# Kernel optimization log

Measured on AMD Instinct MI355X. Metric: run time of the kernel, lower is better.

The kernel has to match this reference:

```python
import jax, jax.numpy as jnp
import numpy as np

B, QL, KL, D, H = 2, 512, 8192, 1024, 8
HD = D // H  # head dim = 128


def setup_inputs() -> dict:
    key = jax.random.key(0)
    ks = jax.random.split(key, 12)
    s = 0.02
    return {
        "inputs_q": jax.random.normal(ks[0], (B, QL, D), jnp.float32),
        "inputs_k": jax.random.normal(ks[1], (B, KL, D), jnp.float32),
        "inputs_v": jax.random.normal(ks[2], (B, KL, D), jnp.float32),
        "attention_mask": jax.random.randint(ks[3], (B, QL, KL), 0, 2).astype(bool),
        "Wq": jax.random.normal(ks[4], (D, D), jnp.float32) * s,
        "bq": jnp.zeros((D,), jnp.float32),
        "Wk": jax.random.normal(ks[5], (D, D), jnp.float32) * s,
        "bk": jnp.zeros((D,), jnp.float32),
        "Wv": jax.random.normal(ks[6], (D, D), jnp.float32) * s,
        "bv": jnp.zeros((D,), jnp.float32),
        "Wf": jax.random.normal(ks[7], (D, D), jnp.float32) * s,
        "bf": jnp.zeros((D,), jnp.float32),
    }


def reference(inputs_q, inputs_k, inputs_v, attention_mask, Wq, bq, Wk, bk, Wv, bv, Wf, bf):
    # Projections (torch Linear: x @ W.T + b)
    q = inputs_q @ Wq.T + bq  # [B, QL, D]
    k = inputs_k @ Wk.T + bk  # [B, KL, D]
    v = inputs_v @ Wv.T + bv  # [B, KL, D]

    q = q.reshape(B, QL, H, HD)
    k = k.reshape(B, KL, H, HD)
    v = v.reshape(B, KL, H, HD)

    # scores [B, H, QL, KL]
    scores = jnp.einsum("bqhd,bkhd->bhqk", q, k)
    scale = 1.0 / np.sqrt(HD).astype(np.float32)
    scores = scores * scale
    large_k = jnp.float32(1e30)
    scores = jnp.where(attention_mask[:, None, :, :], scores, -large_k)

    probs = jax.nn.softmax(scores, axis=-1)
    # note: original calls self.dropout(normalized) but discards the result -> no-op

    summed = jnp.einsum("bhqk,bkhd->bqhd", probs, v).reshape(B, QL, H * HD)

    # wipe rows whose mask is all zero
    wipe = jnp.all(~attention_mask, axis=2, keepdims=True)  # [B, QL, 1]
    summed = jnp.where(wipe, jnp.zeros_like(summed), summed)

    return summed @ Wf.T + bf
```

## Files before the change

### kernel.cpp

```cpp
#include <hip/hip_runtime.h>
#include <hip/hip_bf16.h>
#include <math.h>

typedef __attribute__((ext_vector_type(4))) float fx4;
typedef __attribute__((ext_vector_type(4))) short sx4;
typedef __attribute__((ext_vector_type(8))) short sx8;
typedef unsigned long long u64;

#define MFMA16(a, b, c) __builtin_amdgcn_mfma_f32_16x16x16bf16_1k(a, b, c, 0, 0, 0)
#define MFMA32(a, b, c) __builtin_amdgcn_mfma_f32_16x16x32_bf16(a, b, c, 0, 0, 0)

__device__ __forceinline__ unsigned short f2bf(float f) {
  unsigned int u = __float_as_uint(f);
  return (unsigned short)((u + 0x7fffu + ((u >> 16) & 1u)) >> 16);
}

typedef const __attribute__((address_space(1))) char* gc1p;
typedef __attribute__((address_space(3))) char* lc3p;
__device__ __forceinline__ void glds16(const void* g, const void* lds_uniform) {
  gc1p gp = (gc1p)(unsigned long long)(uintptr_t)g;
  lc3p lp = (lc3p)(unsigned)__builtin_amdgcn_readfirstlane((int)(unsigned)(uintptr_t)lds_uniform);
  __builtin_amdgcn_global_load_lds(gp, lp, 16, 0, 0);
}

__global__ __launch_bounds__(256) void k_conv(const float* __restrict__ s,
                                              short* __restrict__ d) {
  size_t i = ((size_t)blockIdx.x * 256 + threadIdx.x) * 8;
  const fx4 a = *(const fx4*)(s + i);
  const fx4 b = *(const fx4*)(s + i + 4);
  sx8 o;
  o[0] = (short)f2bf(a[0]); o[1] = (short)f2bf(a[1]);
  o[2] = (short)f2bf(a[2]); o[3] = (short)f2bf(a[3]);
  o[4] = (short)f2bf(b[0]); o[5] = (short)f2bf(b[1]);
  o[6] = (short)f2bf(b[2]); o[7] = (short)f2bf(b[3]);
  *(sx8*)(d + i) = o;
}

__global__ __launch_bounds__(256) void k_conv_a(const float* ink, const float* inq,
                                                const float* Wq, const float* Wk,
                                                const float* Wv, const float* Wf,
                                                short* ck, short* cq, short* cwq,
                                                short* cwk, short* cwv, short* cwf) {
  int bx = blockIdx.x;
  const float* s;
  short* d;
  size_t i;
  if (bx < 8192) {
    s = ink; d = ck; i = (size_t)bx * 2048;
  } else {
    const int r = bx - 8192;
    const int seg = r >> 9;
    s = seg == 0 ? inq : seg == 1 ? Wq : seg == 2 ? Wk : seg == 3 ? Wv : Wf;
    d = seg == 0 ? cq : seg == 1 ? cwq : seg == 2 ? cwk : seg == 3 ? cwv : cwf;
    i = (size_t)(r & 511) * 2048;
  }
  i += (size_t)threadIdx.x * 8;
  const fx4 a = *(const fx4*)(s + i);
  const fx4 b = *(const fx4*)(s + i + 4);
  sx8 o;
  o[0] = (short)f2bf(a[0]); o[1] = (short)f2bf(a[1]);
  o[2] = (short)f2bf(a[2]); o[3] = (short)f2bf(a[3]);
  o[4] = (short)f2bf(b[0]); o[5] = (short)f2bf(b[1]);
  o[6] = (short)f2bf(b[2]); o[7] = (short)f2bf(b[3]);
  *(sx8*)(d + i) = o;
}

__global__ __launch_bounds__(256) void k_pack_mask(const int* __restrict__ mask,
                                                   u64* __restrict__ mb) {
  int g = blockIdx.x * 256 + threadIdx.x;
  u64 bal = __ballot(mask[g] != 0);
  if ((threadIdx.x & 63) == 0) mb[g >> 6] = bal;
}

template <int MODE>
__global__ __launch_bounds__(256) void k_gemm(const short* __restrict__ A,
                                              const short* __restrict__ Bw,
                                              const float* __restrict__ bias,
                                              void* __restrict__ Cptr,
                                              int M, int N, int K, float alpha) {
  __shared__ __align__(16) short sA[8192];
  __shared__ __align__(16) short sB[8192];
  const int t = threadIdx.x;
  const int lane = t & 63;
  const int w = t >> 6;
  const int quad = lane >> 4;
  const int l16 = lane & 15;
  const int x7 = l16 & 7;
  const int ntile = N >> 7;
  const int n0 = (blockIdx.x % ntile) << 7;
  const int m0 = (blockIdx.x / ntile) << 7;
  const int wm = (w >> 1) << 6;
  const int wn = (w & 1) << 6;
  const fx4 fzero = {0.f, 0.f, 0.f, 0.f};
  fx4 acc[4][4];
#pragma unroll
  for (int i = 0; i < 4; i++)
#pragma unroll
    for (int j = 0; j < 4; j++) acc[i][j] = fzero;

  const int srow = (lane >> 3);
  const int scb = lane & 7;

  for (int k0 = 0; k0 < K; k0 += 64) {
    __syncthreads();
#pragma unroll
    for (int j = 0; j < 4; j++) {
      const int row = w * 32 + j * 8 + srow;
      const int cb = scb ^ (row & 7);
      glds16(A + (size_t)(m0 + row) * K + k0 + cb * 8, &sA[(w * 32 + j * 8) * 64]);
      glds16(Bw + (size_t)(n0 + row) * K + k0 + cb * 8, &sB[(w * 32 + j * 8) * 64]);
    }
    __syncthreads();
#pragma unroll
    for (int kc = 0; kc < 2; kc++) {
      const int cbp = ((kc * 4 + quad) ^ x7) * 8;
      sx8 fa[4], fb[4];
#pragma unroll
      for (int i = 0; i < 4; i++) {
        fa[i] = *(const sx8*)(&sA[(wm + i * 16 + l16) * 64 + cbp]);
        fb[i] = *(const sx8*)(&sB[(wn + i * 16 + l16) * 64 + cbp]);
      }
#pragma unroll
      for (int mi = 0; mi < 4; mi++)
#pragma unroll
        for (int ni = 0; ni < 4; ni++)
          acc[mi][ni] = MFMA32(fa[mi], fb[ni], acc[mi][ni]);
    }
  }
#pragma unroll
  for (int ni = 0; ni < 4; ni++) {
    const int col = n0 + wn + ni * 16 + l16;
    const float bval = bias[col];
    if (MODE == 2) {
#pragma unroll
      for (int mi = 0; mi < 4; mi++) {
        const int rowb = m0 + wm + mi * 16 + quad * 4;
        const int bb = rowb >> 13;
        const int kl = (rowb & 8191) ^ ((col & 8) ? 4 : 0);
        sx4 pkv;
#pragma unroll
        for (int r = 0; r < 4; r++) pkv[r] = (short)f2bf(acc[mi][ni][r] + bval);
        *(sx4*)((unsigned short*)Cptr + ((size_t)bb * 1024 + col) * 8192 + kl) = pkv;
      }
    } else {
#pragma unroll
      for (int mi = 0; mi < 4; mi++)
#pragma unroll
        for (int r = 0; r < 4; r++) {
          const int row = m0 + wm + mi * 16 + quad * 4 + r;
          const float v = (acc[mi][ni][r] + bval) * alpha;
          if (MODE == 1) ((float*)Cptr)[(size_t)row * N + col] = v;
          else ((unsigned short*)Cptr)[(size_t)row * N + col] = f2bf(v);
        }
    }
  }
}

__global__ __launch_bounds__(256, 4) void k_attn(const short* __restrict__ Qp,
                                                 const short* __restrict__ Kp,
                                                 const short* __restrict__ Vt,
                                                 const u64* __restrict__ mb,
                                                 float* __restrict__ ml,
                                                 float* __restrict__ Op) {
  __shared__ __align__(16) short sK[8192];
  __shared__ __align__(16) short sV[8192];
  const int x = blockIdx.x;
  const int s = x & 7;
  const int qt = (x >> 3) & 7;
  const int h = (x >> 6) & 7;
  const int b = x >> 9;
  const int t = threadIdx.x;
  const int lane = t & 63;
  const int w = t >> 6;
  const int quad = lane >> 4;
  const int l16 = lane & 15;
  const int x7 = l16 & 7;
  const int q0 = qt << 6;
  const fx4 fzero = {0.f, 0.f, 0.f, 0.f};

  const short* qbase = Qp + (size_t)(b * 512 + q0 + w * 16 + l16) * 1024 + h * 128;
  sx8 aq[4];
#pragma unroll
  for (int kc = 0; kc < 4; kc++) aq[kc] = *(const sx8*)(qbase + kc * 32 + quad * 8);

  fx4 Ot[8];
#pragma unroll
  for (int d = 0; d < 8; d++) Ot[d] = fzero;
  float lsum = 0.f;

  const short* kbase = Kp + (size_t)(b * 8192 + s * 1024) * 1024 + h * 128;
  const short* vbase = Vt + (size_t)(b * 1024 + h * 128) * 8192 + s * 1024;
  const u64* wdp = mb + (size_t)(b * 512 + q0 + w * 16 + l16) * 128 + s * 16;
  const int srow4 = lane >> 4, scb16 = lane & 15;
  const int srow8 = lane >> 3, scb8 = lane & 7;
  const int h4 = ((quad & 1) ^ ((l16 >> 3) & 1)) * 4;

  for (int kt = 0; kt < 16; kt++) {
    __syncthreads();
#pragma unroll
    for (int j = 0; j < 4; j++) {
      const int row = (w * 4 + j) * 4 + srow4;
      const int cb = scb16 ^ (row & 7);
      glds16(kbase + (size_t)(kt * 64 + row) * 1024 + cb * 8, &sK[(w * 4 + j) * 512]);
    }
#pragma unroll
    for (int j = 0; j < 4; j++) {
      const int row = (w * 4 + j) * 8 + srow8;
      const int cb = scb8 ^ (row & 7);
      glds16(vbase + (size_t)row * 8192 + kt * 64 + cb * 8, &sV[(w * 4 + j) * 512]);
    }
    const u64 wd = wdp[kt];
    __syncthreads();
    const unsigned lo = (unsigned)wd, hi = (unsigned)(wd >> 32);
    sx4 pk[4];
#pragma unroll
    for (int nt = 0; nt < 4; nt++) {
      fx4 a = fzero;
#pragma unroll
      for (int kc = 0; kc < 4; kc++) {
        const sx8 kf = *(const sx8*)(&sK[(nt * 16 + l16) * 128 + ((kc * 4 + quad) ^ x7) * 8]);
        a = MFMA32(kf, aq[kc], a);
      }
      const unsigned bits = (nt & 2) ? hi : lo;
      const int sh = (nt & 1) * 16 + quad * 4;
      float pv[4];
#pragma unroll
      for (int r = 0; r < 4; r++) {
        const float e = __builtin_amdgcn_exp2f(a[r]);
        pv[r] = ((bits >> (sh + r)) & 1u) ? e : 0.f;
        lsum += pv[r];
      }
      sx4 pko;
      ((unsigned*)&pko)[0] = __builtin_amdgcn_perm(
          __float_as_uint(pv[1]) + 0x8000u, __float_as_uint(pv[0]) + 0x8000u, 0x07060302u);
      ((unsigned*)&pko)[1] = __builtin_amdgcn_perm(
          __float_as_uint(pv[3]) + 0x8000u, __float_as_uint(pv[2]) + 0x8000u, 0x07060302u);
      pk[nt] = pko;
    }
#pragma unroll
    for (int dt = 0; dt < 8; dt++) {
      fx4 o = Ot[dt];
#pragma unroll
      for (int nt = 0; nt < 4; nt++) {
        const int cb = (2 * nt + (quad >> 1)) ^ x7;
        const sx4 vf = *(const sx4*)(&sV[(dt * 16 + l16) * 64 + cb * 8 + h4]);
        o = MFMA16(vf, pk[nt], o);
      }
      Ot[dt] = o;
    }
  }
  lsum += __shfl_xor(lsum, 16, 64);
  lsum += __shfl_xor(lsum, 32, 64);
  if (lane < 16) ml[(size_t)x * 64 + w * 16 + l16] = lsum;
  float* ob = Op + (size_t)x * 8192 + (w * 16 + l16) * 128 + quad * 4;
#pragma unroll
  for (int dt = 0; dt < 8; dt++) *(fx4*)(ob + dt * 16) = Ot[dt];
}

__global__ __launch_bounds__(256) void k_combine(const float* __restrict__ ml,
                                                 const float* __restrict__ Op,
                                                 short* __restrict__ summed) {
  const int xc = blockIdx.x;
  const int qt = xc & 7;
  const int h = (xc >> 3) & 7;
  const int b = xc >> 6;
  const int t = threadIdx.x;
  const int row = t >> 2;
  const int dg = (t & 3) * 32;
  float L = 0.f;
#pragma unroll
  for (int s = 0; s < 8; s++) L += ml[(size_t)(xc * 8 + s) * 64 + row];
  float o[32];
#pragma unroll
  for (int i = 0; i < 32; i++) o[i] = 0.f;
  if (L != 0.f) {
#pragma unroll
    for (int s = 0; s < 8; s++) {
      const float* src = Op + (size_t)(xc * 8 + s) * 8192 + row * 128 + dg;
#pragma unroll
      for (int i = 0; i < 8; i++) {
        const fx4 v = *(const fx4*)(src + i * 4);
        o[i * 4 + 0] += v[0]; o[i * 4 + 1] += v[1];
        o[i * 4 + 2] += v[2]; o[i * 4 + 3] += v[3];
      }
    }
    const float inv = 1.f / L;
#pragma unroll
    for (int i = 0; i < 32; i++) o[i] *= inv;
  }
  short* dst = summed + (size_t)(b * 512 + qt * 64 + row) * 1024 + h * 128 + dg;
#pragma unroll
  for (int i = 0; i < 4; i++) {
    sx8 pkv;
#pragma unroll
    for (int j = 0; j < 8; j++) pkv[j] = (short)f2bf(o[i * 8 + j]);
    *(sx8*)(dst + i * 8) = pkv;
  }
}

extern "C" void kernel_launch(void* const* d_in, const int* in_sizes, int n_in,
                              void* d_out, int out_size, void* d_ws, size_t ws_size,
                              hipStream_t stream) {
  (void)in_sizes; (void)n_in; (void)out_size; (void)ws_size;
  const float* inq = (const float*)d_in[0];
  const float* ink = (const float*)d_in[1];
  const float* inv = (const float*)d_in[2];
  const int* mask = (const int*)d_in[3];
  const float* Wq = (const float*)d_in[4];
  const float* bq = (const float*)d_in[5];
  const float* Wk = (const float*)d_in[6];
  const float* bk = (const float*)d_in[7];
  const float* Wv = (const float*)d_in[8];
  const float* bv = (const float*)d_in[9];
  const float* Wf = (const float*)d_in[10];
  const float* bf = (const float*)d_in[11];

  char* ws = (char*)d_ws;
  short* S1 = (short*)(ws + 0);
  short* S2 = (short*)(ws + 33554432);
  short* S3 = (short*)(ws + 67108864);
  short* cq = (short*)(ws + 100663296);
  short* cwq = (short*)(ws + 102760448);
  short* cwk = (short*)(ws + 104857600);
  short* cwv = (short*)(ws + 106954752);
  short* cwf = (short*)(ws + 109051904);
  short* Qp = (short*)(ws + 111149056);
  short* summed = (short*)(ws + 113246208);
  u64* mb = (u64*)(ws + 115343360);
  float* ml = (float*)(ws + 116391936);

  const float alpha_q = 0.12751757f;

  k_conv_a<<<10752, 256, 0, stream>>>(ink, inq, Wq, Wk, Wv, Wf, S1, cq, cwq, cwk, cwv, cwf);
  k_pack_mask<<<32768, 256, 0, stream>>>(mask, mb);
  k_gemm<0><<<1024, 256, 0, stream>>>(S1, cwk, bk, S2, 16384, 1024, 1024, 1.f);
  k_conv<<<8192, 256, 0, stream>>>(inv, S1);
  k_gemm<2><<<1024, 256, 0, stream>>>(S1, cwv, bv, S3, 16384, 1024, 1024, 1.f);
  k_gemm<0><<<64, 256, 0, stream>>>(cq, cwq, bq, Qp, 1024, 1024, 1024, alpha_q);
  k_attn<<<1024, 256, 0, stream>>>(Qp, S2, S3, mb, ml, (float*)S1);
  k_combine<<<128, 256, 0, stream>>>(ml, (const float*)S1, summed);
  k_gemm<1><<<64, 256, 0, stream>>>(summed, cwf, bf, (float*)d_out, 1024, 1024, 1024, 1.f);
}
```

Before: 428.1 us.

## Fuse fp32-to-bf16 conversion into GEMM A loads and remap block orders

The projection GEMMs now read fp32 activations directly, prefetching the next K tile into registers and converting to bf16 when storing to LDS. This removes the separate conversion passes over the large K and V inputs and their bf16 round-trip through memory. The mask packing now uses vectorized int4 loads with an LDS nibble gather, and the large GEMM and the attention kernel get remapped block orders aimed at better L2 locality. The cost is register-staged A loads that lose the direct global-to-LDS path and double the A read bytes.

```diff
diff --git a/kernel.cpp b/kernel.cpp
--- a/kernel.cpp
+++ b/kernel.cpp
@@ -13,6 +13,13 @@
 __device__ __forceinline__ unsigned short f2bf(float f) {
   unsigned int u = __float_as_uint(f);
   return (unsigned short)((u + 0x7fffu + ((u >> 16) & 1u)) >> 16);
+}
+
+__device__ __forceinline__ sx4 pk4(const fx4 v) {
+  sx4 o;
+  o[0] = (short)f2bf(v[0]); o[1] = (short)f2bf(v[1]);
+  o[2] = (short)f2bf(v[2]); o[3] = (short)f2bf(v[3]);
+  return o;
 }
 
 typedef const __attribute__((address_space(1))) char* gc1p;
@@ -23,9 +30,14 @@
   __builtin_amdgcn_global_load_lds(gp, lp, 16, 0, 0);
 }
 
-__global__ __launch_bounds__(256) void k_conv(const float* __restrict__ s,
-                                              short* __restrict__ d) {
-  size_t i = ((size_t)blockIdx.x * 256 + threadIdx.x) * 8;
+__global__ __launch_bounds__(256) void k_conv4(const float* s0, const float* s1,
+                                               const float* s2, const float* s3,
+                                               short* d0, short* d1, short* d2,
+                                               short* d3) {
+  const int seg = blockIdx.x >> 9;
+  const float* s = seg == 0 ? s0 : seg == 1 ? s1 : seg == 2 ? s2 : s3;
+  short* d = seg == 0 ? d0 : seg == 1 ? d1 : seg == 2 ? d2 : d3;
+  size_t i = (size_t)(blockIdx.x & 511) * 2048 + (size_t)threadIdx.x * 8;
   const fx4 a = *(const fx4*)(s + i);
   const fx4 b = *(const fx4*)(s + i + 4);
   sx8 o;
@@ -36,44 +48,24 @@
   *(sx8*)(d + i) = o;
 }
 
-__global__ __launch_bounds__(256) void k_conv_a(const float* ink, const float* inq,
-                                                const float* Wq, const float* Wk,
-                                                const float* Wv, const float* Wf,
-                                                short* ck, short* cq, short* cwq,
-                                                short* cwk, short* cwv, short* cwf) {
-  int bx = blockIdx.x;
-  const float* s;
-  short* d;
-  size_t i;
-  if (bx < 8192) {
-    s = ink; d = ck; i = (size_t)bx * 2048;
-  } else {
-    const int r = bx - 8192;
-    const int seg = r >> 9;
-    s = seg == 0 ? inq : seg == 1 ? Wq : seg == 2 ? Wk : seg == 3 ? Wv : Wf;
-    d = seg == 0 ? cq : seg == 1 ? cwq : seg == 2 ? cwk : seg == 3 ? cwv : cwf;
-    i = (size_t)(r & 511) * 2048;
-  }
-  i += (size_t)threadIdx.x * 8;
-  const fx4 a = *(const fx4*)(s + i);
-  const fx4 b = *(const fx4*)(s + i + 4);
-  sx8 o;
-  o[0] = (short)f2bf(a[0]); o[1] = (short)f2bf(a[1]);
-  o[2] = (short)f2bf(a[2]); o[3] = (short)f2bf(a[3]);
-  o[4] = (short)f2bf(b[0]); o[5] = (short)f2bf(b[1]);
-  o[6] = (short)f2bf(b[2]); o[7] = (short)f2bf(b[3]);
-  *(sx8*)(d + i) = o;
-}
-
 __global__ __launch_bounds__(256) void k_pack_mask(const int* __restrict__ mask,
                                                    u64* __restrict__ mb) {
-  int g = blockIdx.x * 256 + threadIdx.x;
-  u64 bal = __ballot(mask[g] != 0);
-  if ((threadIdx.x & 63) == 0) mb[g >> 6] = bal;
-}
-
-template <int MODE>
-__global__ __launch_bounds__(256) void k_gemm(const short* __restrict__ A,
+  __shared__ unsigned char nib[256];
+  const int t = threadIdx.x;
+  const int4 m = *(const int4*)(mask + (size_t)blockIdx.x * 1024 + t * 4);
+  nib[t] = (unsigned char)((m.x != 0) | ((m.y != 0) << 1) | ((m.z != 0) << 2) |
+                           ((m.w != 0) << 3));
+  __syncthreads();
+  if (t < 16) {
+    u64 wv = 0;
+#pragma unroll
+    for (int i = 0; i < 16; i++) wv |= (u64)(nib[t * 16 + i] & 0xF) << (4 * i);
+    mb[(size_t)blockIdx.x * 16 + t] = wv;
+  }
+}
+
+template <int MODE, bool AF32>
+__global__ __launch_bounds__(256) void k_gemm(const void* __restrict__ Aptr,
                                               const short* __restrict__ Bw,
                                               const float* __restrict__ bias,
                                               void* __restrict__ Cptr,
@@ -86,9 +78,16 @@
   const int quad = lane >> 4;
   const int l16 = lane & 15;
   const int x7 = l16 & 7;
-  const int ntile = N >> 7;
-  const int n0 = (blockIdx.x % ntile) << 7;
-  const int m0 = (blockIdx.x / ntile) << 7;
+  int m0, n0;
+  if (M >= 8192) {
+    const int ml = blockIdx.x & 7, nn = (blockIdx.x >> 3) & 7, mh = blockIdx.x >> 6;
+    m0 = (mh * 8 + ml) << 7;
+    n0 = nn << 7;
+  } else {
+    const int ntile = N >> 7;
+    n0 = (blockIdx.x % ntile) << 7;
+    m0 = (blockIdx.x / ntile) << 7;
+  }
   const int wm = (w >> 1) << 6;
   const int wn = (w & 1) << 6;
   const fx4 fzero = {0.f, 0.f, 0.f, 0.f};
@@ -100,17 +99,48 @@
 
   const int srow = (lane >> 3);
   const int scb = lane & 7;
+  const float* Af = (const float*)Aptr;
+  const int arow = t >> 4;
+  const int acol = (t & 15) * 4;
+  const int acb = ((t & 15) >> 1) ^ (arow & 7);
+  const int ahalf = ((t & 15) & 1) * 4;
+  fx4 areg[8];
+  if (AF32) {
+#pragma unroll
+    for (int p = 0; p < 8; p++)
+      areg[p] = *(const fx4*)(Af + (size_t)(m0 + arow + p * 16) * K + acol);
+  }
 
   for (int k0 = 0; k0 < K; k0 += 64) {
     __syncthreads();
+    if (AF32) {
+#pragma unroll
+      for (int p = 0; p < 8; p++) {
+        const int row = arow + p * 16;
+        *(sx4*)(&sA[row * 64 + acb * 8 + ahalf]) = pk4(areg[p]);
+      }
+    } else {
+      const short* Ab = (const short*)Aptr;
+#pragma unroll
+      for (int j = 0; j < 4; j++) {
+        const int row = w * 32 + j * 8 + srow;
+        const int cb = scb ^ (row & 7);
+        glds16(Ab + (size_t)(m0 + row) * K + k0 + cb * 8, &sA[(w * 32 + j * 8) * 64]);
+      }
+    }
 #pragma unroll
     for (int j = 0; j < 4; j++) {
       const int row = w * 32 + j * 8 + srow;
       const int cb = scb ^ (row & 7);
-      glds16(A + (size_t)(m0 + row) * K + k0 + cb * 8, &sA[(w * 32 + j * 8) * 64]);
       glds16(Bw + (size_t)(n0 + row) * K + k0 + cb * 8, &sB[(w * 32 + j * 8) * 64]);
     }
     __syncthreads();
+    if (AF32) {
+      const int kn = (k0 + 64 < K) ? k0 + 64 : k0;
+#pragma unroll
+      for (int p = 0; p < 8; p++)
+        areg[p] = *(const fx4*)(Af + (size_t)(m0 + arow + p * 16) * K + kn + acol);
+    }
 #pragma unroll
     for (int kc = 0; kc < 2; kc++) {
       const int cbp = ((kc * 4 + quad) ^ x7) * 8;
@@ -165,10 +195,14 @@
   __shared__ __align__(16) short sK[8192];
   __shared__ __align__(16) short sV[8192];
   const int x = blockIdx.x;
-  const int s = x & 7;
+  const int gl = x & 7;
   const int qt = (x >> 3) & 7;
-  const int h = (x >> 6) & 7;
-  const int b = x >> 9;
+  const int gh = x >> 6;
+  const int g = gh * 8 + gl;
+  const int s = g & 7;
+  const int h = (g >> 3) & 7;
+  const int b = g >> 6;
+  const int li = ((b * 8 + h) * 8 + qt) * 8 + s;
   const int t = threadIdx.x;
   const int lane = t & 63;
   const int w = t >> 6;
@@ -251,8 +285,8 @@
   }
   lsum += __shfl_xor(lsum, 16, 64);
   lsum += __shfl_xor(lsum, 32, 64);
-  if (lane < 16) ml[(size_t)x * 64 + w * 16 + l16] = lsum;
-  float* ob = Op + (size_t)x * 8192 + (w * 16 + l16) * 128 + quad * 4;
+  if (lane < 16) ml[(size_t)li * 64 + w * 16 + l16] = lsum;
+  float* ob = Op + (size_t)li * 8192 + (w * 16 + l16) * 128 + quad * 4;
 #pragma unroll
   for (int dt = 0; dt < 8; dt++) *(fx4*)(ob + dt * 16) = Ot[dt];
 }
@@ -316,28 +350,26 @@
   const float* bf = (const float*)d_in[11];
 
   char* ws = (char*)d_ws;
-  short* S1 = (short*)(ws + 0);
-  short* S2 = (short*)(ws + 33554432);
-  short* S3 = (short*)(ws + 67108864);
-  short* cq = (short*)(ws + 100663296);
-  short* cwq = (short*)(ws + 102760448);
-  short* cwk = (short*)(ws + 104857600);
-  short* cwv = (short*)(ws + 106954752);
-  short* cwf = (short*)(ws + 109051904);
-  short* Qp = (short*)(ws + 111149056);
-  short* summed = (short*)(ws + 113246208);
-  u64* mb = (u64*)(ws + 115343360);
-  float* ml = (float*)(ws + 116391936);
+  float* Op = (float*)(ws + 0);
+  short* Kp = (short*)(ws + 33554432);
+  short* Vt = (short*)(ws + 67108864);
+  short* cwq = (short*)(ws + 100663296);
+  short* cwk = (short*)(ws + 102760448);
+  short* cwv = (short*)(ws + 104857600);
+  short* cwf = (short*)(ws + 106954752);
+  short* Qp = (short*)(ws + 109051904);
+  short* summed = (short*)(ws + 111149056);
+  u64* mb = (u64*)(ws + 113246208);
+  float* ml = (float*)(ws + 114294784);
 
   const float alpha_q = 0.12751757f;
 
-  k_conv_a<<<10752, 256, 0, stream>>>(ink, inq, Wq, Wk, Wv, Wf, S1, cq, cwq, cwk, cwv, cwf);
-  k_pack_mask<<<32768, 256, 0, stream>>>(mask, mb);
-  k_gemm<0><<<1024, 256, 0, stream>>>(S1, cwk, bk, S2, 16384, 1024, 1024, 1.f);
-  k_conv<<<8192, 256, 0, stream>>>(inv, S1);
-  k_gemm<2><<<1024, 256, 0, stream>>>(S1, cwv, bv, S3, 16384, 1024, 1024, 1.f);
-  k_gemm<0><<<64, 256, 0, stream>>>(cq, cwq, bq, Qp, 1024, 1024, 1024, alpha_q);
-  k_attn<<<1024, 256, 0, stream>>>(Qp, S2, S3, mb, ml, (float*)S1);
-  k_combine<<<128, 256, 0, stream>>>(ml, (const float*)S1, summed);
-  k_gemm<1><<<64, 256, 0, stream>>>(summed, cwf, bf, (float*)d_out, 1024, 1024, 1024, 1.f);
-}
+  k_conv4<<<2048, 256, 0, stream>>>(Wq, Wk, Wv, Wf, cwq, cwk, cwv, cwf);
+  k_pack_mask<<<8192, 256, 0, stream>>>(mask, mb);
+  k_gemm<0, true><<<1024, 256, 0, stream>>>(ink, cwk, bk, Kp, 16384, 1024, 1024, 1.f);
+  k_gemm<2, true><<<1024, 256, 0, stream>>>(inv, cwv, bv, Vt, 16384, 1024, 1024, 1.f);
+  k_gemm<0, true><<<64, 256, 0, stream>>>(inq, cwq, bq, Qp, 1024, 1024, 1024, alpha_q);
+  k_attn<<<1024, 256, 0, stream>>>(Qp, Kp, Vt, mb, ml, Op);
+  k_combine<<<128, 256, 0, stream>>>(ml, Op, summed);
+  k_gemm<1, false><<<64, 256, 0, stream>>>(summed, cwf, bf, (float*)d_out, 1024, 1024, 1024, 1.f);
+}
```

Result: slower. 439.4 us (+2.6%).
